# Kernel optimization log

Hardware: AMD Instinct MI355X
Metric: run time of the kernel (lower is better)

The kernel has to match this reference:

```python
import jax, jax.numpy as jnp
import numpy as np

N, IN_DIM, OUT_DIM, H = 8192, 512, 512, 1
BN_EPS = 1e-5


def _lin(key, fan_in, fan_out):
    k1, k2 = jax.random.split(key)
    b = 1.0 / np.sqrt(fan_in)
    W = jax.random.uniform(k1, (fan_in, fan_out), jnp.float32, -b, b)
    bias = jax.random.uniform(k2, (fan_out,), jnp.float32, -b, b)
    return W, bias


def setup_inputs() -> dict:
    key = jax.random.key(0)
    ks = jax.random.split(key, 12)
    h = jax.random.normal(ks[0], (N, IN_DIM), jnp.float32)
    A = (jax.random.uniform(ks[1], (N, N)) < 0.01).astype(jnp.float32)
    qw, qb = _lin(ks[2], IN_DIM, OUT_DIM * H)
    kw, kb = _lin(ks[3], IN_DIM, OUT_DIM * H)
    vw, vb = _lin(ks[4], IN_DIM, OUT_DIM * H)
    ow, ob = _lin(ks[5], OUT_DIM, OUT_DIM)
    f1w, f1b = _lin(ks[6], OUT_DIM, OUT_DIM * 2)
    f2w, f2b = _lin(ks[7], OUT_DIM * 2, OUT_DIM)
    bn1_g = jax.random.normal(ks[8], (OUT_DIM,)) * 0.1 + 1.0
    bn1_b = jax.random.normal(ks[9], (OUT_DIM,)) * 0.1
    bn1_m = jax.random.normal(ks[10], (OUT_DIM,)) * 0.1
    bn1_v = jax.random.uniform(ks[11], (OUT_DIM,), jnp.float32, 0.5, 1.5)
    ks2 = jax.random.split(jax.random.fold_in(key, 7), 4)
    bn2_g = jax.random.normal(ks2[0], (OUT_DIM,)) * 0.1 + 1.0
    bn2_b = jax.random.normal(ks2[1], (OUT_DIM,)) * 0.1
    bn2_m = jax.random.normal(ks2[2], (OUT_DIM,)) * 0.1
    bn2_v = jax.random.uniform(ks2[3], (OUT_DIM,), jnp.float32, 0.5, 1.5)
    return dict(A=A, h=h, qw=qw, qb=qb, kw=kw, kb=kb, vw=vw, vb=vb,
                ow=ow, ob=ob, f1w=f1w, f1b=f1b, f2w=f2w, f2b=f2b,
                bn1_g=bn1_g, bn1_b=bn1_b, bn1_m=bn1_m, bn1_v=bn1_v,
                bn2_g=bn2_g, bn2_b=bn2_b, bn2_m=bn2_m, bn2_v=bn2_v)


def _bn_eval(x, g, b, m, v):
    return (x - m) * jax.lax.rsqrt(v + BN_EPS) * g + b


def reference(A, h, qw, qb, kw, kb, vw, vb, ow, ob, f1w, f1b, f2w, f2b,
              bn1_g, bn1_b, bn1_m, bn1_v, bn2_g, bn2_b, bn2_m, bn2_v):
    n = h.shape[0]
    scaling = OUT_DIM ** (-0.5)
    # q/k/v: [N, D, H] as in torch reshape of [N, D*H]
    q = (h @ qw + qb).reshape(n, OUT_DIM, H) * scaling
    k = (h @ kw + kb).reshape(n, OUT_DIM, H)
    v = (h @ vw + vb).reshape(n, OUT_DIM, H)
    qh = jnp.transpose(q, (2, 0, 1))          # (H, N, D)
    kh = jnp.transpose(k, (2, 1, 0))          # (H, D, N)
    vh = jnp.transpose(v, (2, 0, 1))          # (H, N, D)
    attn = jnp.einsum('hnd,hdm->hnm', qh, kh) * A[None]   # (H, N, N)
    attn = jax.nn.softmax(attn, axis=0)        # NOTE: softmax over HEAD axis, as in source
    out = jnp.einsum('hnm,hmd->hnd', attn, vh).reshape(n, H * OUT_DIM)
    # GTLayer (eval mode: dropout = identity, BN uses running stats)
    x = out @ ow + ob
    x = x + h                                  # residual
    x = _bn_eval(x, bn1_g, bn1_b, bn1_m, bn1_v)
    h2 = x
    f = jax.nn.relu(x @ f1w + f1b) @ f2w + f2b
    x = h2 + f
    x = _bn_eval(x, bn2_g, bn2_b, bn2_m, bn2_v)
    return x
```

## Files before the change

kernel.cpp:

```cpp
#include <hip/hip_runtime.h>

#define NROWS 8192
#define DIM 512
#define HID 1024
#define BN_EPS 1e-5f

typedef unsigned short ushort_t;
typedef __attribute__((ext_vector_type(8))) __bf16 bf16x8;
typedef __attribute__((ext_vector_type(4))) float f32x4;

union U4 {
    uint4 u;
    bf16x8 b;
    ushort_t s[8];
};

static __device__ __forceinline__ float b2f(ushort_t u) {
    union { float f; unsigned int i; } c;
    c.i = ((unsigned int)u) << 16;
    return c.f;
}

static __device__ __forceinline__ ushort_t f2b(float f) {
    union { float f; unsigned int i; } c;
    c.f = f;
    unsigned int i = c.i;
    unsigned int r = (i + 0x7FFFu + ((i >> 16) & 1u)) >> 16;
    return (ushort_t)r;
}

__global__ void colsum_kernel(const float* __restrict__ h, float* __restrict__ hs) {
    int t = threadIdx.x;
    int col0 = (t & 127) * 4;
    int rsub = t >> 7;
    int row0 = blockIdx.x * 128;
    float acc[4] = {0.f, 0.f, 0.f, 0.f};
    for (int r = 0; r < 64; ++r) {
        int row = row0 + r * 2 + rsub;
        float4 v = *(const float4*)(h + row * DIM + col0);
        acc[0] += v.x; acc[1] += v.y; acc[2] += v.z; acc[3] += v.w;
    }
#pragma unroll
    for (int j = 0; j < 4; ++j) atomicAdd(&hs[col0 + j], acc[j]);
}

__global__ void matvec_kernel(const float* __restrict__ xin, const float* __restrict__ W,
                              const float* __restrict__ bvec, float scaleB,
                              float* __restrict__ outv) {
    __shared__ float red[8][32];
    int t = threadIdx.x;
    int col = blockIdx.x * 32 + (t & 31);
    int ks = t >> 5;
    float s = 0.f;
    for (int ki = 0; ki < 64; ++ki) {
        int k = ks * 64 + ki;
        s += xin[k] * W[k * 512 + col];
    }
    red[ks][t & 31] = s;
    __syncthreads();
    if (ks == 0) {
        float tot = scaleB * bvec[col];
#pragma unroll
        for (int r = 0; r < 8; ++r) tot += red[r][t & 31];
        outv[col] = tot;
    }
}

__global__ void prep_const_kernel(const float* __restrict__ tvec,
                                  const float* g1, const float* b1,
                                  const float* m1, const float* v1,
                                  const float* g2, const float* b2,
                                  const float* m2, const float* v2,
                                  float* __restrict__ p, float* __restrict__ q0,
                                  float* __restrict__ a2v, float* __restrict__ c2v) {
    int d = threadIdx.x;
    float a1 = g1[d] * rsqrtf(v1[d] + BN_EPS);
    float c1 = b1[d] - m1[d] * a1;
    p[d] = a1;
    q0[d] = tvec[d] * a1 + c1;
    float a2 = g2[d] * rsqrtf(v2[d] + BN_EPS);
    a2v[d] = a2;
    c2v[d] = b2[d] - m2[d] * a2;
}

__global__ void x1_kernel(const float* __restrict__ h, const float* __restrict__ p,
                          const float* __restrict__ q0, ushort_t* __restrict__ x1) {
    int idx = (blockIdx.x * blockDim.x + threadIdx.x) * 4;
    int d0 = idx & (DIM - 1);
    float4 hv = *(const float4*)(h + idx);
    ushort_t ov[4];
    ov[0] = f2b(hv.x * p[d0 + 0] + q0[d0 + 0]);
    ov[1] = f2b(hv.y * p[d0 + 1] + q0[d0 + 1]);
    ov[2] = f2b(hv.z * p[d0 + 2] + q0[d0 + 2]);
    ov[3] = f2b(hv.w * p[d0 + 3] + q0[d0 + 3]);
    *(uint2*)(x1 + idx) = *(uint2*)ov;
}

__global__ void transpose_kernel(const float* __restrict__ in, ushort_t* __restrict__ out,
                                 int R, int C) {
    __shared__ float tile[32][33];
    int tx = threadIdx.x & 31, ty = threadIdx.x >> 5;
    int bx = blockIdx.x * 32, by = blockIdx.y * 32;
#pragma unroll
    for (int i = 0; i < 32; i += 8)
        tile[ty + i][tx] = in[(by + ty + i) * C + bx + tx];
    __syncthreads();
#pragma unroll
    for (int i = 0; i < 32; i += 8)
        out[(bx + ty + i) * R + by + tx] = f2b(tile[tx][ty + i]);
}

template <bool RELU>
__global__ __launch_bounds__(256) void gemm_kernel(const ushort_t* __restrict__ A,
                                                   const ushort_t* __restrict__ BT,
                                                   const float* __restrict__ bias,
                                                   ushort_t* __restrict__ C, int M, int Nn, int K) {
    const int BK = 32, LDA = BK + 8;
    __shared__ ushort_t As[128 * LDA];
    __shared__ ushort_t Bs[128 * LDA];
    int tid = threadIdx.x;
    int lane = tid & 63, w = tid >> 6;
    int wm = (w & 1) * 64, wn = (w >> 1) * 64;
    int bm = blockIdx.y * 128, bn = blockIdx.x * 128;

    f32x4 acc[4][4] = {};

    int c0 = tid, c1 = tid + 256;
    int r0 = c0 >> 2, kc0 = (c0 & 3) * 8;
    int r1 = c1 >> 2, kc1 = (c1 & 3) * 8;

    for (int k0 = 0; k0 < K; k0 += BK) {
        __syncthreads();
        uint4 a0 = *(const uint4*)(A + (size_t)(bm + r0) * K + k0 + kc0);
        uint4 a1 = *(const uint4*)(A + (size_t)(bm + r1) * K + k0 + kc1);
        uint4 b0 = *(const uint4*)(BT + (size_t)(bn + r0) * K + k0 + kc0);
        uint4 b1 = *(const uint4*)(BT + (size_t)(bn + r1) * K + k0 + kc1);
        *(uint4*)(As + r0 * LDA + kc0) = a0;
        *(uint4*)(As + r1 * LDA + kc1) = a1;
        *(uint4*)(Bs + r0 * LDA + kc0) = b0;
        *(uint4*)(Bs + r1 * LDA + kc1) = b1;
        __syncthreads();

        int koff = (lane >> 4) * 8;
        bf16x8 af[4], bfr[4];
#pragma unroll
        for (int i = 0; i < 4; ++i) {
            U4 t;
            t.u = *(const uint4*)(As + (wm + i * 16 + (lane & 15)) * LDA + koff);
            af[i] = t.b;
        }
#pragma unroll
        for (int j = 0; j < 4; ++j) {
            U4 t;
            t.u = *(const uint4*)(Bs + (wn + j * 16 + (lane & 15)) * LDA + koff);
            bfr[j] = t.b;
        }
#pragma unroll
        for (int i = 0; i < 4; ++i)
#pragma unroll
            for (int j = 0; j < 4; ++j)
                acc[i][j] = __builtin_amdgcn_mfma_f32_16x16x32_bf16(af[i], bfr[j], acc[i][j], 0, 0, 0);
    }

#pragma unroll
    for (int i = 0; i < 4; ++i) {
        int row0 = bm + wm + i * 16 + (lane >> 4) * 4;
#pragma unroll
        for (int j = 0; j < 4; ++j) {
            int col = bn + wn + j * 16 + (lane & 15);
            float bv = bias[col];
#pragma unroll
            for (int r = 0; r < 4; ++r) {
                float v = acc[i][j][r] + bv;
                if (RELU) v = fmaxf(v, 0.f);
                C[(size_t)(row0 + r) * Nn + col] = f2b(v);
            }
        }
    }
}

__global__ void final_kernel(const float* __restrict__ h, const ushort_t* __restrict__ F,
                             const float* __restrict__ p, const float* __restrict__ q0,
                             const float* __restrict__ a2v, const float* __restrict__ c2v,
                             float* __restrict__ out) {
    int idx = (blockIdx.x * blockDim.x + threadIdx.x) * 4;
    int d0 = idx & (DIM - 1);
    float4 hv = *(const float4*)(h + idx);
    ushort_t fv[4];
    *(uint2*)fv = *(const uint2*)(F + idx);
    float4 ov;
    ov.x = ((hv.x * p[d0 + 0] + q0[d0 + 0]) + b2f(fv[0])) * a2v[d0 + 0] + c2v[d0 + 0];
    ov.y = ((hv.y * p[d0 + 1] + q0[d0 + 1]) + b2f(fv[1])) * a2v[d0 + 1] + c2v[d0 + 1];
    ov.z = ((hv.z * p[d0 + 2] + q0[d0 + 2]) + b2f(fv[2])) * a2v[d0 + 2] + c2v[d0 + 2];
    ov.w = ((hv.w * p[d0 + 3] + q0[d0 + 3]) + b2f(fv[3])) * a2v[d0 + 3] + c2v[d0 + 3];
    *(float4*)(out + idx) = ov;
}

extern "C" void kernel_launch(void* const* d_in, const int* in_sizes, int n_in,
                              void* d_out, int out_size, void* d_ws, size_t ws_size,
                              hipStream_t stream) {
    const float* h = (const float*)d_in[1];
    const float* vw = (const float*)d_in[6];
    const float* vb = (const float*)d_in[7];
    const float* ow = (const float*)d_in[8];
    const float* ob = (const float*)d_in[9];
    const float* f1w = (const float*)d_in[10];
    const float* f1b = (const float*)d_in[11];
    const float* f2w = (const float*)d_in[12];
    const float* f2b = (const float*)d_in[13];
    const float* g1 = (const float*)d_in[14];
    const float* b1 = (const float*)d_in[15];
    const float* m1 = (const float*)d_in[16];
    const float* v1 = (const float*)d_in[17];
    const float* g2 = (const float*)d_in[18];
    const float* b2 = (const float*)d_in[19];
    const float* m2 = (const float*)d_in[20];
    const float* v2 = (const float*)d_in[21];
    float* out = (float*)d_out;

    char* ws = (char*)d_ws;
    float* hs = (float*)(ws + 0);
    float* pC = (float*)(ws + 2048);
    float* q0C = (float*)(ws + 4096);
    float* a2C = (float*)(ws + 6144);
    float* c2C = (float*)(ws + 8192);
    float* sBuf = (float*)(ws + 10240);
    float* tBuf = (float*)(ws + 12288);
    ushort_t* X1 = (ushort_t*)(ws + 16384);
    ushort_t* Z = X1 + (size_t)NROWS * DIM;
    ushort_t* F = Z + (size_t)NROWS * HID;
    ushort_t* W1T = F + (size_t)NROWS * DIM;
    ushort_t* W2T = W1T + (size_t)HID * DIM;

    hipMemsetAsync(hs, 0, 512 * sizeof(float), stream);
    colsum_kernel<<<64, 256, 0, stream>>>(h, hs);
    matvec_kernel<<<16, 256, 0, stream>>>(hs, vw, vb, 8192.0f, sBuf);
    matvec_kernel<<<16, 256, 0, stream>>>(sBuf, ow, ob, 1.0f, tBuf);
    prep_const_kernel<<<1, 512, 0, stream>>>(tBuf, g1, b1, m1, v1, g2, b2, m2, v2,
                                             pC, q0C, a2C, c2C);
    x1_kernel<<<4096, 256, 0, stream>>>(h, pC, q0C, X1);
    transpose_kernel<<<dim3(32, 16), 256, 0, stream>>>(f1w, W1T, 512, 1024);
    transpose_kernel<<<dim3(16, 32), 256, 0, stream>>>(f2w, W2T, 1024, 512);
    gemm_kernel<true><<<dim3(8, 64), 256, 0, stream>>>(X1, W1T, f1b, Z, NROWS, HID, DIM);
    gemm_kernel<false><<<dim3(4, 64), 256, 0, stream>>>(Z, W2T, f2b, F, NROWS, DIM, HID);
    final_kernel<<<4096, 256, 0, stream>>>(h, F, pC, q0C, a2C, c2C, out);
}
```

Measured before the change: 434.7 us.

## Fold BN1 affine into W1 and fuse residual/BN2 epilogue into second GEMM

The BN1 scale is folded into a transposed, scaled copy of W1, and the shift is folded into a new bias computed by a matvec. This lets the first GEMM read raw fp32 h directly and convert it to bf16 in-kernel, removing the separate x1 pass and its buffer. The second GEMM now uses a 128x64 tile and applies the residual and BN2 in its epilogue, writing fp32 output directly and dropping the F buffer and final kernel. Colsum uses more, smaller blocks. The trade-offs are fp32 A loads in gemm1 with in-loop conversion, uncoalesced strided h reads in the gemm2 epilogue, and a slightly different rounding point.

```diff
diff --git a/kernel.cpp b/kernel.cpp
--- a/kernel.cpp
+++ b/kernel.cpp
@@ -33,11 +33,11 @@
     int t = threadIdx.x;
     int col0 = (t & 127) * 4;
     int rsub = t >> 7;
-    int row0 = blockIdx.x * 128;
+    int row0 = blockIdx.x * 32;
     float acc[4] = {0.f, 0.f, 0.f, 0.f};
-    for (int r = 0; r < 64; ++r) {
+    for (int r = 0; r < 16; ++r) {
         int row = row0 + r * 2 + rsub;
-        float4 v = *(const float4*)(h + row * DIM + col0);
+        float4 v = *(const float4*)(h + (size_t)row * DIM + col0);
         acc[0] += v.x; acc[1] += v.y; acc[2] += v.z; acc[3] += v.w;
     }
 #pragma unroll
@@ -46,7 +46,7 @@
 
 __global__ void matvec_kernel(const float* __restrict__ xin, const float* __restrict__ W,
                               const float* __restrict__ bvec, float scaleB,
-                              float* __restrict__ outv) {
+                              float* __restrict__ outv, int ncols) {
     __shared__ float red[8][32];
     int t = threadIdx.x;
     int col = blockIdx.x * 32 + (t & 31);
@@ -54,7 +54,7 @@
     float s = 0.f;
     for (int ki = 0; ki < 64; ++ki) {
         int k = ks * 64 + ki;
-        s += xin[k] * W[k * 512 + col];
+        s += xin[k] * W[(size_t)k * ncols + col];
     }
     red[ks][t & 31] = s;
     __syncthreads();
@@ -83,17 +83,18 @@
     c2v[d] = b2[d] - m2[d] * a2;
 }
 
-__global__ void x1_kernel(const float* __restrict__ h, const float* __restrict__ p,
-                          const float* __restrict__ q0, ushort_t* __restrict__ x1) {
-    int idx = (blockIdx.x * blockDim.x + threadIdx.x) * 4;
-    int d0 = idx & (DIM - 1);
-    float4 hv = *(const float4*)(h + idx);
-    ushort_t ov[4];
-    ov[0] = f2b(hv.x * p[d0 + 0] + q0[d0 + 0]);
-    ov[1] = f2b(hv.y * p[d0 + 1] + q0[d0 + 1]);
-    ov[2] = f2b(hv.z * p[d0 + 2] + q0[d0 + 2]);
-    ov[3] = f2b(hv.w * p[d0 + 3] + q0[d0 + 3]);
-    *(uint2*)(x1 + idx) = *(uint2*)ov;
+__global__ void scaleT_kernel(const float* __restrict__ in, const float* __restrict__ p,
+                              ushort_t* __restrict__ out, int R, int C) {
+    __shared__ float tile[32][33];
+    int tx = threadIdx.x & 31, ty = threadIdx.x >> 5;
+    int bx = blockIdx.x * 32, by = blockIdx.y * 32;
+#pragma unroll
+    for (int i = 0; i < 32; i += 8)
+        tile[ty + i][tx] = in[(size_t)(by + ty + i) * C + bx + tx];
+    __syncthreads();
+#pragma unroll
+    for (int i = 0; i < 32; i += 8)
+        out[(size_t)(bx + ty + i) * R + by + tx] = f2b(tile[tx][ty + i] * p[by + tx]);
 }
 
 __global__ void transpose_kernel(const float* __restrict__ in, ushort_t* __restrict__ out,
@@ -103,19 +104,18 @@
     int bx = blockIdx.x * 32, by = blockIdx.y * 32;
 #pragma unroll
     for (int i = 0; i < 32; i += 8)
-        tile[ty + i][tx] = in[(by + ty + i) * C + bx + tx];
+        tile[ty + i][tx] = in[(size_t)(by + ty + i) * C + bx + tx];
     __syncthreads();
 #pragma unroll
     for (int i = 0; i < 32; i += 8)
-        out[(bx + ty + i) * R + by + tx] = f2b(tile[tx][ty + i]);
-}
-
-template <bool RELU>
-__global__ __launch_bounds__(256) void gemm_kernel(const ushort_t* __restrict__ A,
-                                                   const ushort_t* __restrict__ BT,
-                                                   const float* __restrict__ bias,
-                                                   ushort_t* __restrict__ C, int M, int Nn, int K) {
-    const int BK = 32, LDA = BK + 8;
+        out[(size_t)(bx + ty + i) * R + by + tx] = f2b(tile[tx][ty + i]);
+}
+
+__global__ __launch_bounds__(256) void gemm1_kernel(const float* __restrict__ A,
+                                                    const ushort_t* __restrict__ BT,
+                                                    const float* __restrict__ bias,
+                                                    ushort_t* __restrict__ C) {
+    const int K = DIM, Nn = HID, BK = 32, LDA = BK + 8;
     __shared__ ushort_t As[128 * LDA];
     __shared__ ushort_t Bs[128 * LDA];
     int tid = threadIdx.x;
@@ -125,20 +125,28 @@
 
     f32x4 acc[4][4] = {};
 
-    int c0 = tid, c1 = tid + 256;
-    int r0 = c0 >> 2, kc0 = (c0 & 3) * 8;
-    int r1 = c1 >> 2, kc1 = (c1 & 3) * 8;
+    int ra = tid >> 1, kca = (tid & 1) * 16;
+    int r0 = tid >> 2, kc0 = (tid & 3) * 8;
+    int r1 = r0 + 64;
 
     for (int k0 = 0; k0 < K; k0 += BK) {
         __syncthreads();
-        uint4 a0 = *(const uint4*)(A + (size_t)(bm + r0) * K + k0 + kc0);
-        uint4 a1 = *(const uint4*)(A + (size_t)(bm + r1) * K + k0 + kc1);
+        const float* ap = A + (size_t)(bm + ra) * K + k0 + kca;
+        float4 fa = *(const float4*)(ap + 0);
+        float4 fb = *(const float4*)(ap + 4);
+        float4 fc = *(const float4*)(ap + 8);
+        float4 fd = *(const float4*)(ap + 12);
         uint4 b0 = *(const uint4*)(BT + (size_t)(bn + r0) * K + k0 + kc0);
-        uint4 b1 = *(const uint4*)(BT + (size_t)(bn + r1) * K + k0 + kc1);
-        *(uint4*)(As + r0 * LDA + kc0) = a0;
-        *(uint4*)(As + r1 * LDA + kc1) = a1;
+        uint4 b1 = *(const uint4*)(BT + (size_t)(bn + r1) * K + k0 + kc0);
+        ushort_t av[16];
+        av[0] = f2b(fa.x); av[1] = f2b(fa.y); av[2] = f2b(fa.z); av[3] = f2b(fa.w);
+        av[4] = f2b(fb.x); av[5] = f2b(fb.y); av[6] = f2b(fb.z); av[7] = f2b(fb.w);
+        av[8] = f2b(fc.x); av[9] = f2b(fc.y); av[10] = f2b(fc.z); av[11] = f2b(fc.w);
+        av[12] = f2b(fd.x); av[13] = f2b(fd.y); av[14] = f2b(fd.z); av[15] = f2b(fd.w);
+        *(uint4*)(As + ra * LDA + kca) = *(uint4*)(av);
+        *(uint4*)(As + ra * LDA + kca + 8) = *(uint4*)(av + 8);
         *(uint4*)(Bs + r0 * LDA + kc0) = b0;
-        *(uint4*)(Bs + r1 * LDA + kc1) = b1;
+        *(uint4*)(Bs + r1 * LDA + kc0) = b1;
         __syncthreads();
 
         int koff = (lane >> 4) * 8;
@@ -171,29 +179,82 @@
             float bv = bias[col];
 #pragma unroll
             for (int r = 0; r < 4; ++r) {
-                float v = acc[i][j][r] + bv;
-                if (RELU) v = fmaxf(v, 0.f);
+                float v = fmaxf(acc[i][j][r] + bv, 0.f);
                 C[(size_t)(row0 + r) * Nn + col] = f2b(v);
             }
         }
     }
 }
 
-__global__ void final_kernel(const float* __restrict__ h, const ushort_t* __restrict__ F,
-                             const float* __restrict__ p, const float* __restrict__ q0,
-                             const float* __restrict__ a2v, const float* __restrict__ c2v,
-                             float* __restrict__ out) {
-    int idx = (blockIdx.x * blockDim.x + threadIdx.x) * 4;
-    int d0 = idx & (DIM - 1);
-    float4 hv = *(const float4*)(h + idx);
-    ushort_t fv[4];
-    *(uint2*)fv = *(const uint2*)(F + idx);
-    float4 ov;
-    ov.x = ((hv.x * p[d0 + 0] + q0[d0 + 0]) + b2f(fv[0])) * a2v[d0 + 0] + c2v[d0 + 0];
-    ov.y = ((hv.y * p[d0 + 1] + q0[d0 + 1]) + b2f(fv[1])) * a2v[d0 + 1] + c2v[d0 + 1];
-    ov.z = ((hv.z * p[d0 + 2] + q0[d0 + 2]) + b2f(fv[2])) * a2v[d0 + 2] + c2v[d0 + 2];
-    ov.w = ((hv.w * p[d0 + 3] + q0[d0 + 3]) + b2f(fv[3])) * a2v[d0 + 3] + c2v[d0 + 3];
-    *(float4*)(out + idx) = ov;
+__global__ __launch_bounds__(256) void gemm2_kernel(const ushort_t* __restrict__ A,
+                                                    const ushort_t* __restrict__ BT,
+                                                    const float* __restrict__ bias,
+                                                    const float* __restrict__ h,
+                                                    const float* __restrict__ p,
+                                                    const float* __restrict__ q0,
+                                                    const float* __restrict__ a2v,
+                                                    const float* __restrict__ c2v,
+                                                    float* __restrict__ out) {
+    const int K = HID, BK = 32, LDA = BK + 8;
+    __shared__ ushort_t As[128 * LDA];
+    __shared__ ushort_t Bs[64 * LDA];
+    int tid = threadIdx.x;
+    int lane = tid & 63, w = tid >> 6;
+    int wm = (w & 1) * 64, wn = (w >> 1) * 32;
+    int bm = blockIdx.y * 128, bn = blockIdx.x * 64;
+
+    f32x4 acc[4][2] = {};
+
+    int r0 = tid >> 2, kc0 = (tid & 3) * 8;
+    int r1 = r0 + 64;
+
+    for (int k0 = 0; k0 < K; k0 += BK) {
+        __syncthreads();
+        uint4 a0 = *(const uint4*)(A + (size_t)(bm + r0) * K + k0 + kc0);
+        uint4 a1 = *(const uint4*)(A + (size_t)(bm + r1) * K + k0 + kc0);
+        uint4 bb = *(const uint4*)(BT + (size_t)(bn + r0) * K + k0 + kc0);
+        *(uint4*)(As + r0 * LDA + kc0) = a0;
+        *(uint4*)(As + r1 * LDA + kc0) = a1;
+        *(uint4*)(Bs + r0 * LDA + kc0) = bb;
+        __syncthreads();
+
+        int koff = (lane >> 4) * 8;
+        bf16x8 af[4], bfr[2];
+#pragma unroll
+        for (int i = 0; i < 4; ++i) {
+            U4 t;
+            t.u = *(const uint4*)(As + (wm + i * 16 + (lane & 15)) * LDA + koff);
+            af[i] = t.b;
+        }
+#pragma unroll
+        for (int j = 0; j < 2; ++j) {
+            U4 t;
+            t.u = *(const uint4*)(Bs + (wn + j * 16 + (lane & 15)) * LDA + koff);
+            bfr[j] = t.b;
+        }
+#pragma unroll
+        for (int i = 0; i < 4; ++i)
+#pragma unroll
+            for (int j = 0; j < 2; ++j)
+                acc[i][j] = __builtin_amdgcn_mfma_f32_16x16x32_bf16(af[i], bfr[j], acc[i][j], 0, 0, 0);
+    }
+
+#pragma unroll
+    for (int i = 0; i < 4; ++i) {
+        int row0 = bm + wm + i * 16 + (lane >> 4) * 4;
+#pragma unroll
+        for (int j = 0; j < 2; ++j) {
+            int col = bn + wn + j * 16 + (lane & 15);
+            float bv = bias[col], pp = p[col], qq = q0[col];
+            float aa = a2v[col], cc = c2v[col];
+#pragma unroll
+            for (int r = 0; r < 4; ++r) {
+                int row = row0 + r;
+                float x1 = h[(size_t)row * DIM + col] * pp + qq;
+                out[(size_t)row * DIM + col] = (x1 + acc[i][j][r] + bv) * aa + cc;
+            }
+        }
+    }
 }
 
 extern "C" void kernel_launch(void* const* d_in, const int* in_sizes, int n_in,
@@ -207,7 +268,7 @@
     const float* f1w = (const float*)d_in[10];
     const float* f1b = (const float*)d_in[11];
     const float* f2w = (const float*)d_in[12];
-    const float* f2b = (const float*)d_in[13];
+    const float* fb2 = (const float*)d_in[13];
     const float* g1 = (const float*)d_in[14];
     const float* b1 = (const float*)d_in[15];
     const float* m1 = (const float*)d_in[16];
@@ -226,22 +287,20 @@
     float* c2C = (float*)(ws + 8192);
     float* sBuf = (float*)(ws + 10240);
     float* tBuf = (float*)(ws + 12288);
-    ushort_t* X1 = (ushort_t*)(ws + 16384);
-    ushort_t* Z = X1 + (size_t)NROWS * DIM;
-    ushort_t* F = Z + (size_t)NROWS * HID;
-    ushort_t* W1T = F + (size_t)NROWS * DIM;
-    ushort_t* W2T = W1T + (size_t)HID * DIM;
+    float* b1P = (float*)(ws + 16384);
+    ushort_t* W1T = (ushort_t*)(ws + 32768);
+    ushort_t* W2T = (ushort_t*)(ws + 32768 + 1048576);
+    ushort_t* Z = (ushort_t*)(ws + 32768 + 2097152);
 
     hipMemsetAsync(hs, 0, 512 * sizeof(float), stream);
-    colsum_kernel<<<64, 256, 0, stream>>>(h, hs);
-    matvec_kernel<<<16, 256, 0, stream>>>(hs, vw, vb, 8192.0f, sBuf);
-    matvec_kernel<<<16, 256, 0, stream>>>(sBuf, ow, ob, 1.0f, tBuf);
+    colsum_kernel<<<256, 256, 0, stream>>>(h, hs);
+    matvec_kernel<<<16, 256, 0, stream>>>(hs, vw, vb, 8192.0f, sBuf, 512);
+    matvec_kernel<<<16, 256, 0, stream>>>(sBuf, ow, ob, 1.0f, tBuf, 512);
     prep_const_kernel<<<1, 512, 0, stream>>>(tBuf, g1, b1, m1, v1, g2, b2, m2, v2,
                                              pC, q0C, a2C, c2C);
-    x1_kernel<<<4096, 256, 0, stream>>>(h, pC, q0C, X1);
-    transpose_kernel<<<dim3(32, 16), 256, 0, stream>>>(f1w, W1T, 512, 1024);
+    matvec_kernel<<<32, 256, 0, stream>>>(q0C, f1w, f1b, 1.0f, b1P, 1024);
+    scaleT_kernel<<<dim3(32, 16), 256, 0, stream>>>(f1w, pC, W1T, 512, 1024);
     transpose_kernel<<<dim3(16, 32), 256, 0, stream>>>(f2w, W2T, 1024, 512);
-    gemm_kernel<true><<<dim3(8, 64), 256, 0, stream>>>(X1, W1T, f1b, Z, NROWS, HID, DIM);
-    gemm_kernel<false><<<dim3(4, 64), 256, 0, stream>>>(Z, W2T, f2b, F, NROWS, DIM, HID);
-    final_kernel<<<4096, 256, 0, stream>>>(h, F, pC, q0C, a2C, c2C, out);
-}
+    gemm1_kernel<<<dim3(8, 64), 256, 0, stream>>>(h, W1T, b1P, Z);
+    gemm2_kernel<<<dim3(8, 64), 256, 0, stream>>>(Z, W2T, fb2, h, pC, q0C, a2C, c2C, out);
+}
```

Result: slower. 478.7 us (+10.1%).
